# Kernel tuning notes

Measured on AMD Instinct MI355X. Metric: run time of the kernel, lower is better.

## Reference

```python
import jax, jax.numpy as jnp
import numpy as np

N = 50000
E = 600000
IN_C = 128
HID_C = 128
OUT_C = 128


def _glorot(key, shape):
    fan_in, fan_out = shape[0], shape[1]
    lim = np.sqrt(6.0 / (fan_in + fan_out))
    return jax.random.uniform(key, shape, jnp.float32, -lim, lim)


def setup_inputs() -> dict:
    key = jax.random.key(0)
    ks = jax.random.split(key, 10)
    x = jax.random.normal(ks[0], (N, IN_C), jnp.float32)
    edge_index = jax.random.randint(ks[1], (2, E), 0, N, jnp.int64)
    return {
        "x": x,
        "edge_index": edge_index,
        # SAGEConv1: lin_l (aggregated, with bias) and lin_r (root, no bias)
        "W1_l": _glorot(ks[2], (IN_C, HID_C)),
        "b1_l": jnp.zeros((HID_C,), jnp.float32),
        "W1_r": _glorot(ks[3], (IN_C, HID_C)),
        # SAGEConv2
        "W2_l": _glorot(ks[4], (HID_C, OUT_C)),
        "b2_l": jnp.zeros((OUT_C,), jnp.float32),
        "W2_r": _glorot(ks[5], (HID_C, OUT_C)),
        # final Linear(hidden+out -> out)
        "W_lin": _glorot(ks[6], (HID_C + OUT_C, OUT_C)),
        "b_lin": jnp.zeros((OUT_C,), jnp.float32),
    }


def _sage_conv(x, src, dst, W_l, b_l, W_r):
    # mean-aggregate source features onto destination nodes
    msg = x[src]                                   # [E, C] gather
    agg = jax.ops.segment_sum(msg, dst, num_segments=N)        # [N, C]
    cnt = jax.ops.segment_sum(jnp.ones((src.shape[0],), x.dtype), dst,
                              num_segments=N)                   # [N]
    mean = agg / jnp.maximum(cnt, 1.0)[:, None]
    return mean @ W_l + b_l + x @ W_r


def reference(x, edge_index, W1_l, b1_l, W1_r, W2_l, b2_l, W2_r, W_lin, b_lin):
    src, dst = edge_index[0], edge_index[1]
    x1 = jax.nn.relu(_sage_conv(x, src, dst, W1_l, b1_l, W1_r))   # [N, HID]
    x2 = jax.nn.relu(_sage_conv(x1, src, dst, W2_l, b2_l, W2_r))  # [N, OUT]
    return jnp.concatenate([x1, x2], axis=-1) @ W_lin + b_lin     # [N, OUT]
```

## Files before the change

kernel.cpp:

```cpp
#include <hip/hip_runtime.h>


typedef _Float16 f16;
typedef __attribute__((ext_vector_type(2))) _Float16 f16x2;
typedef __attribute__((ext_vector_type(4))) _Float16 f16x4;
typedef __attribute__((ext_vector_type(8))) _Float16 f16x8;
typedef __attribute__((ext_vector_type(4))) float f32x4;

__global__ void convert_f32_to_f16(const float* __restrict__ in, f16* __restrict__ out, int n4) {
  int i = blockIdx.x * blockDim.x + threadIdx.x;
  if (i < n4) {
    const float4 v = ((const float4*)in)[i];
    f16x4 h = { (f16)v.x, (f16)v.y, (f16)v.z, (f16)v.w };
    ((f16x4*)out)[i] = h;
  }
}

__global__ void prep_w(const float* __restrict__ WA, const float* __restrict__ WB,
                       f16* __restrict__ wt) {
  int tid = blockIdx.x * blockDim.x + threadIdx.x;
  if (tid < 32768) {
    int j = tid & 7, n = (tid >> 3) & 127, chunk = tid >> 10;
    int k = chunk * 8 + j;
    float v = (k < 128) ? WA[k * 128 + n] : WB[(k - 128) * 128 + n];
    wt[tid] = (f16)v;
  }
}

__global__ void deg_kernel(const int* __restrict__ ei, int* __restrict__ deg, int E) {
  int e = blockIdx.x * blockDim.x + threadIdx.x;
  if (e < E) atomicAdd(&deg[ei[E + e]], 1);
}

__global__ void scan_block_kernel(const int* __restrict__ in, int* __restrict__ out,
                                  int* __restrict__ sums, int n) {
  __shared__ int s[2][1024];
  int t = threadIdx.x;
  int gid = blockIdx.x * 1024 + t;
  int v = (gid < n) ? in[gid] : 0;
  int cur = 0;
  s[0][t] = v;
  __syncthreads();
  for (int ofs = 1; ofs < 1024; ofs <<= 1) {
    int nv = s[cur][t] + ((t >= ofs) ? s[cur][t - ofs] : 0);
    s[cur ^ 1][t] = nv;
    cur ^= 1;
    __syncthreads();
  }
  if (gid < n) out[gid] = s[cur][t] - v;
  if (t == 1023) sums[blockIdx.x] = s[cur][1023];
}

__global__ void scan_sums_kernel(int* __restrict__ sums, int nb, int* __restrict__ off, int n) {
  int lane = threadIdx.x;
  int orig = (lane < nb) ? sums[lane] : 0;
  int v = orig;
  for (int ofs = 1; ofs < 64; ofs <<= 1) {
    int u = __shfl_up(v, ofs);
    if (lane >= ofs) v += u;
  }
  if (lane < nb) sums[lane] = v - orig;
  if (lane == nb - 1) off[n] = v;
}

__global__ void scan_add_kernel(int* __restrict__ off, const int* __restrict__ sums, int n) {
  int gid = blockIdx.x * 1024 + threadIdx.x;
  if (gid < n) off[gid] += sums[blockIdx.x];
}

__global__ void fill_kernel(const int* __restrict__ ei, const int* __restrict__ off,
                            int* __restrict__ cursor, int* __restrict__ srcs, int E) {
  int e = blockIdx.x * blockDim.x + threadIdx.x;
  if (e < E) {
    int src = ei[e], dst = ei[E + e];
    int pos = atomicAdd(&cursor[dst], 1);
    srcs[off[dst] + pos] = src;
  }
}

__global__ void aggregate_kernel(const f16* __restrict__ feat, const int* __restrict__ off,
                                 const int* __restrict__ srcs, f16* __restrict__ meanf, int n) {
  int wid = (int)((blockIdx.x * blockDim.x + threadIdx.x) >> 6);
  int lane = threadIdx.x & 63;
  if (wid >= n) return;
  int sub = lane >> 4, n15 = lane & 15;
  int beg = off[wid], end = off[wid + 1];
  int deg = end - beg;
  float acc[8] = {};
  int e = beg;
  int bulkEnd = beg + (deg & ~7);
  for (; e < bulkEnd; e += 8) {
    int sA = srcs[e + sub];
    int sB = srcs[e + 4 + sub];
    f16x8 vA = *(const f16x8*)(feat + (size_t)sA * 128 + n15 * 8);
    f16x8 vB = *(const f16x8*)(feat + (size_t)sB * 128 + n15 * 8);
#pragma unroll
    for (int j = 0; j < 8; ++j) acc[j] += (float)vA[j] + (float)vB[j];
  }
  int rem = end - e;
  if (sub < rem) {
    int s = srcs[e + sub];
    f16x8 v = *(const f16x8*)(feat + (size_t)s * 128 + n15 * 8);
#pragma unroll
    for (int j = 0; j < 8; ++j) acc[j] += (float)v[j];
  }
  if (sub + 4 < rem) {
    int s = srcs[e + 4 + sub];
    f16x8 v = *(const f16x8*)(feat + (size_t)s * 128 + n15 * 8);
#pragma unroll
    for (int j = 0; j < 8; ++j) acc[j] += (float)v[j];
  }
#pragma unroll
  for (int j = 0; j < 8; ++j) {
    acc[j] += __shfl_xor(acc[j], 16);
    acc[j] += __shfl_xor(acc[j], 32);
  }
  if (sub == 0) {
    float inv = 1.0f / fmaxf((float)deg, 1.0f);
    f16x8 o;
#pragma unroll
    for (int j = 0; j < 8; ++j) o[j] = (f16)(acc[j] * inv);
    *(f16x8*)(meanf + (size_t)wid * 128 + n15 * 8) = o;
  }
}

template <bool RELU, bool OUT16>
__global__ __launch_bounds__(256, 2) void gemm_kernel(
    const f16* __restrict__ U, const f16* __restrict__ V, const f16* __restrict__ Wt,
    const float* __restrict__ bias, void* __restrict__ outp, int M) {
  __shared__ f16 ldsb[32768];
  int tid = threadIdx.x;
  int wave = tid >> 6, lane = tid & 63;
  int quad = lane >> 4, n15 = lane & 15;
  int m0 = blockIdx.x * 128 + wave * 32;
  int kq = quad * 8;

  f16x8 a[2][8];
#pragma unroll
  for (int r = 0; r < 2; ++r) {
    int row = m0 + r * 16 + n15;
    int rowc = row < M ? row : M - 1;
    const f16* bu = U + (size_t)rowc * 128 + kq;
    const f16* bv = V + (size_t)rowc * 128 + kq;
#pragma unroll
    for (int kk = 0; kk < 4; ++kk) a[r][kk] = *(const f16x8*)(bu + kk * 32);
#pragma unroll
    for (int kk = 4; kk < 8; ++kk) a[r][kk] = *(const f16x8*)(bv + (kk - 4) * 32);
  }

#pragma unroll
  for (int it = 0; it < 16; ++it) {
    int idx = it * 256 + tid;
    ((f16x8*)ldsb)[idx] = ((const f16x8*)Wt)[idx];
  }
  __syncthreads();

  f32x4 acc[2][8] = {};
#pragma unroll
  for (int kk = 0; kk < 8; ++kk) {
#pragma unroll
    for (int t = 0; t < 8; ++t) {
      f16x8 b = ((const f16x8*)ldsb)[(kk * 4 + quad) * 128 + t * 16 + n15];
#pragma unroll
      for (int r = 0; r < 2; ++r)
        acc[r][t] = __builtin_amdgcn_mfma_f32_16x16x32_f16(a[r][kk], b, acc[r][t], 0, 0, 0);
    }
  }

  int rbase0 = m0 + quad * 4;
#pragma unroll
  for (int t = 0; t < 8; ++t) {
    float bv = bias[t * 16 + n15];
#pragma unroll
    for (int r = 0; r < 2; ++r) {
#pragma unroll
      for (int i = 0; i < 4; ++i) {
        int row = rbase0 + r * 16 + i;
        if (row < M) {
          float v = acc[r][t][i] + bv;
          if (RELU) v = fmaxf(v, 0.f);
          size_t idx = (size_t)row * 128 + t * 16 + n15;
          if (OUT16) ((f16*)outp)[idx] = (f16)v;
          else       ((float*)outp)[idx] = v;
        }
      }
    }
  }
}

extern "C" void kernel_launch(void* const* d_in, const int* in_sizes, int n_in,
                              void* d_out, int out_size, void* d_ws, size_t ws_size,
                              hipStream_t stream) {
  (void)n_in; (void)out_size; (void)ws_size;
  const float* x    = (const float*)d_in[0];
  const int*   ei   = (const int*)d_in[1];
  const float* W1l  = (const float*)d_in[2];
  const float* b1l  = (const float*)d_in[3];
  const float* W1r  = (const float*)d_in[4];
  const float* W2l  = (const float*)d_in[5];
  const float* b2l  = (const float*)d_in[6];
  const float* W2r  = (const float*)d_in[7];
  const float* Wlin = (const float*)d_in[8];
  const float* blin = (const float*)d_in[9];
  const int N = in_sizes[0] / 128;
  const int E = in_sizes[1] / 2;

  char* ws = (char*)d_ws;
  size_t o = 0;
  auto alloc = [&](size_t bytes) {
    char* p = ws + o;
    o = (o + bytes + 255) & ~(size_t)255;
    return p;
  };
  f16* xh   = (f16*)alloc((size_t)N * 128 * 2);
  f16* x1h  = (f16*)alloc((size_t)N * 128 * 2);
  f16* x2h  = (f16*)alloc((size_t)N * 128 * 2);
  f16* mh   = (f16*)alloc((size_t)N * 128 * 2);
  f16* wt1  = (f16*)alloc(32768 * 2);
  f16* wt2  = (f16*)alloc(32768 * 2);
  f16* wt3  = (f16*)alloc(32768 * 2);
  int* deg  = (int*)alloc((size_t)N * 2 * 4);
  int* cur  = deg + N;
  int* off  = (int*)alloc(((size_t)N + 1) * 4);
  int* srcs = (int*)alloc((size_t)E * 4);
  int* sums = (int*)alloc(64 * 4);

  hipMemsetAsync(deg, 0, (size_t)N * 2 * 4, stream);

  const int nb = (N + 1023) / 1024;
  deg_kernel<<<(E + 255) / 256, 256, 0, stream>>>(ei, deg, E);
  scan_block_kernel<<<nb, 1024, 0, stream>>>(deg, off, sums, N);
  scan_sums_kernel<<<1, 64, 0, stream>>>(sums, nb, off, N);
  scan_add_kernel<<<nb, 1024, 0, stream>>>(off, sums, N);
  fill_kernel<<<(E + 255) / 256, 256, 0, stream>>>(ei, off, cur, srcs, E);

  convert_f32_to_f16<<<((N * 128 / 4) + 255) / 256, 256, 0, stream>>>(x, xh, N * 128 / 4);
  prep_w<<<128, 256, 0, stream>>>(W1l, W1r, wt1);
  prep_w<<<128, 256, 0, stream>>>(W2l, W2r, wt2);
  prep_w<<<128, 256, 0, stream>>>(Wlin, Wlin + 128 * 128, wt3);

  const int aggBlocks  = (N + 3) / 4;
  const int gemmBlocks = (N + 127) / 128;

  aggregate_kernel<<<aggBlocks, 256, 0, stream>>>(xh, off, srcs, mh, N);
  gemm_kernel<true, true><<<gemmBlocks, 256, 0, stream>>>(mh, xh, wt1, b1l, x1h, N);
  aggregate_kernel<<<aggBlocks, 256, 0, stream>>>(x1h, off, srcs, mh, N);
  gemm_kernel<true, true><<<gemmBlocks, 256, 0, stream>>>(mh, x1h, wt2, b2l, x2h, N);
  gemm_kernel<false, false><<<gemmBlocks, 256, 0, stream>>>(x1h, x2h, wt3, blin, d_out, N);
}
```

Before: 265.1 us.

## Fuse prep kernels, merge scan passes, and batch aggregation two nodes per wave

Merges the x conversion, degree counting and the three weight-repack launches into one multi-role kernel, and folds the scan-sums step into scan_add, which also zeroes the cursor array and writes off[n]=E. This replaces the memset of the cursor and cuts several launches. The aggregation kernel now handles two destination nodes per wave and issues up to six neighbour gathers per node before accumulating, to raise memory-level parallelism. The cost is higher register pressure and more divergence on the remainder path.

```diff
diff --git a/kernel.cpp b/kernel.cpp
--- a/kernel.cpp
+++ b/kernel.cpp
@@ -7,29 +7,34 @@
 typedef __attribute__((ext_vector_type(8))) _Float16 f16x8;
 typedef __attribute__((ext_vector_type(4))) float f32x4;
 
-__global__ void convert_f32_to_f16(const float* __restrict__ in, f16* __restrict__ out, int n4) {
-  int i = blockIdx.x * blockDim.x + threadIdx.x;
-  if (i < n4) {
-    const float4 v = ((const float4*)in)[i];
-    f16x4 h = { (f16)v.x, (f16)v.y, (f16)v.z, (f16)v.w };
-    ((f16x4*)out)[i] = h;
-  }
-}
-
-__global__ void prep_w(const float* __restrict__ WA, const float* __restrict__ WB,
-                       f16* __restrict__ wt) {
-  int tid = blockIdx.x * blockDim.x + threadIdx.x;
-  if (tid < 32768) {
-    int j = tid & 7, n = (tid >> 3) & 127, chunk = tid >> 10;
+__global__ void prep_kernel(const float* __restrict__ x, f16* __restrict__ xh, int n4,
+                            const int* __restrict__ ei, int* __restrict__ deg, int E,
+                            const float* __restrict__ W1l, const float* __restrict__ W1r,
+                            const float* __restrict__ W2l, const float* __restrict__ W2r,
+                            const float* __restrict__ Wlin, f16* __restrict__ wt,
+                            int cb, int db) {
+  int b = blockIdx.x;
+  if (b < cb) {
+    int i = b * 256 + threadIdx.x;
+    if (i < n4) {
+      const float4 v = ((const float4*)x)[i];
+      f16x4 h = { (f16)v.x, (f16)v.y, (f16)v.z, (f16)v.w };
+      ((f16x4*)xh)[i] = h;
+    }
+  } else if (b < cb + db) {
+    int e = (b - cb) * 256 + threadIdx.x;
+    if (e < E) atomicAdd(&deg[ei[E + e]], 1);
+  } else {
+    int tid = (b - cb - db) * 256 + threadIdx.x;
+    int w = tid >> 15, idx = tid & 32767;
+    int j = idx & 7, n = (idx >> 3) & 127, chunk = idx >> 10;
     int k = chunk * 8 + j;
-    float v = (k < 128) ? WA[k * 128 + n] : WB[(k - 128) * 128 + n];
+    float v;
+    if (w == 0) v = (k < 128) ? W1l[k * 128 + n] : W1r[(k - 128) * 128 + n];
+    else if (w == 1) v = (k < 128) ? W2l[k * 128 + n] : W2r[(k - 128) * 128 + n];
+    else v = Wlin[k * 128 + n];
     wt[tid] = (f16)v;
   }
-}
-
-__global__ void deg_kernel(const int* __restrict__ ei, int* __restrict__ deg, int E) {
-  int e = blockIdx.x * blockDim.x + threadIdx.x;
-  if (e < E) atomicAdd(&deg[ei[E + e]], 1);
 }
 
 __global__ void scan_block_kernel(const int* __restrict__ in, int* __restrict__ out,
@@ -51,21 +56,20 @@
   if (t == 1023) sums[blockIdx.x] = s[cur][1023];
 }
 
-__global__ void scan_sums_kernel(int* __restrict__ sums, int nb, int* __restrict__ off, int n) {
-  int lane = threadIdx.x;
-  int orig = (lane < nb) ? sums[lane] : 0;
-  int v = orig;
-  for (int ofs = 1; ofs < 64; ofs <<= 1) {
-    int u = __shfl_up(v, ofs);
-    if (lane >= ofs) v += u;
-  }
-  if (lane < nb) sums[lane] = v - orig;
-  if (lane == nb - 1) off[n] = v;
-}
-
-__global__ void scan_add_kernel(int* __restrict__ off, const int* __restrict__ sums, int n) {
-  int gid = blockIdx.x * 1024 + threadIdx.x;
-  if (gid < n) off[gid] += sums[blockIdx.x];
+__global__ void scan_add_kernel(int* __restrict__ off, const int* __restrict__ sums,
+                                int* __restrict__ cur, int n, int E) {
+  __shared__ int prefix_s;
+  int b = blockIdx.x;
+  if (threadIdx.x < 64) {
+    int v = ((int)threadIdx.x < b) ? sums[threadIdx.x] : 0;
+#pragma unroll
+    for (int ofs = 1; ofs < 64; ofs <<= 1) v += __shfl_xor(v, ofs);
+    if (threadIdx.x == 0) prefix_s = v;
+  }
+  __syncthreads();
+  int gid = b * 1024 + threadIdx.x;
+  if (gid < n) { off[gid] += prefix_s; cur[gid] = 0; }
+  if (gid == 0) off[n] = E;
 }
 
 __global__ void fill_kernel(const int* __restrict__ ei, const int* __restrict__ off,
@@ -78,49 +82,81 @@
   }
 }
 
+#define AGG_R 6
 __global__ void aggregate_kernel(const f16* __restrict__ feat, const int* __restrict__ off,
                                  const int* __restrict__ srcs, f16* __restrict__ meanf, int n) {
-  int wid = (int)((blockIdx.x * blockDim.x + threadIdx.x) >> 6);
+  int pair = (int)((blockIdx.x * blockDim.x + threadIdx.x) >> 6);
+  int w0 = pair * 2;
+  if (w0 >= n) return;
+  int w1 = w0 + 1;
   int lane = threadIdx.x & 63;
-  if (wid >= n) return;
   int sub = lane >> 4, n15 = lane & 15;
-  int beg = off[wid], end = off[wid + 1];
-  int deg = end - beg;
-  float acc[8] = {};
-  int e = beg;
-  int bulkEnd = beg + (deg & ~7);
-  for (; e < bulkEnd; e += 8) {
-    int sA = srcs[e + sub];
-    int sB = srcs[e + 4 + sub];
-    f16x8 vA = *(const f16x8*)(feat + (size_t)sA * 128 + n15 * 8);
-    f16x8 vB = *(const f16x8*)(feat + (size_t)sB * 128 + n15 * 8);
-#pragma unroll
-    for (int j = 0; j < 8; ++j) acc[j] += (float)vA[j] + (float)vB[j];
-  }
-  int rem = end - e;
-  if (sub < rem) {
-    int s = srcs[e + sub];
-    f16x8 v = *(const f16x8*)(feat + (size_t)s * 128 + n15 * 8);
-#pragma unroll
-    for (int j = 0; j < 8; ++j) acc[j] += (float)v[j];
-  }
-  if (sub + 4 < rem) {
-    int s = srcs[e + 4 + sub];
-    f16x8 v = *(const f16x8*)(feat + (size_t)s * 128 + n15 * 8);
-#pragma unroll
-    for (int j = 0; j < 8; ++j) acc[j] += (float)v[j];
+  int beg0 = off[w0], end0 = off[w0 + 1];
+  int beg1 = end0;
+  int end1 = (w1 < n) ? off[w1 + 1] : end0;
+  int deg0 = end0 - beg0, deg1 = end1 - beg1;
+
+  int s0[AGG_R], s1[AGG_R];
+  bool v0[AGG_R], v1[AGG_R];
+#pragma unroll
+  for (int k = 0; k < AGG_R; ++k) {
+    int p = 4 * k + sub;
+    v0[k] = p < deg0;  s0[k] = v0[k] ? srcs[beg0 + p] : 0;
+    v1[k] = p < deg1;  s1[k] = v1[k] ? srcs[beg1 + p] : 0;
+  }
+  f16x8 g0[AGG_R], g1[AGG_R];
+#pragma unroll
+  for (int k = 0; k < AGG_R; ++k) {
+    if (v0[k]) g0[k] = *(const f16x8*)(feat + (size_t)s0[k] * 128 + n15 * 8);
+    if (v1[k]) g1[k] = *(const f16x8*)(feat + (size_t)s1[k] * 128 + n15 * 8);
+  }
+  float acc0[8] = {}, acc1[8] = {};
+#pragma unroll
+  for (int k = 0; k < AGG_R; ++k) {
+    if (v0[k]) {
+#pragma unroll
+      for (int j = 0; j < 8; ++j) acc0[j] += (float)g0[k][j];
+    }
+    if (v1[k]) {
+#pragma unroll
+      for (int j = 0; j < 8; ++j) acc1[j] += (float)g1[k][j];
+    }
+  }
+  for (int e = beg0 + 4 * AGG_R; e < end0; e += 4) {
+    if (sub < end0 - e) {
+      int s = srcs[e + sub];
+      f16x8 g = *(const f16x8*)(feat + (size_t)s * 128 + n15 * 8);
+#pragma unroll
+      for (int j = 0; j < 8; ++j) acc0[j] += (float)g[j];
+    }
+  }
+  for (int e = beg1 + 4 * AGG_R; e < end1; e += 4) {
+    if (sub < end1 - e) {
+      int s = srcs[e + sub];
+      f16x8 g = *(const f16x8*)(feat + (size_t)s * 128 + n15 * 8);
+#pragma unroll
+      for (int j = 0; j < 8; ++j) acc1[j] += (float)g[j];
+    }
   }
 #pragma unroll
   for (int j = 0; j < 8; ++j) {
-    acc[j] += __shfl_xor(acc[j], 16);
-    acc[j] += __shfl_xor(acc[j], 32);
+    acc0[j] += __shfl_xor(acc0[j], 16);
+    acc0[j] += __shfl_xor(acc0[j], 32);
+    acc1[j] += __shfl_xor(acc1[j], 16);
+    acc1[j] += __shfl_xor(acc1[j], 32);
   }
   if (sub == 0) {
-    float inv = 1.0f / fmaxf((float)deg, 1.0f);
+    float inv = 1.0f / fmaxf((float)deg0, 1.0f);
     f16x8 o;
 #pragma unroll
-    for (int j = 0; j < 8; ++j) o[j] = (f16)(acc[j] * inv);
-    *(f16x8*)(meanf + (size_t)wid * 128 + n15 * 8) = o;
+    for (int j = 0; j < 8; ++j) o[j] = (f16)(acc0[j] * inv);
+    *(f16x8*)(meanf + (size_t)w0 * 128 + n15 * 8) = o;
+  } else if (sub == 1 && w1 < n) {
+    float inv = 1.0f / fmaxf((float)deg1, 1.0f);
+    f16x8 o;
+#pragma unroll
+    for (int j = 0; j < 8; ++j) o[j] = (f16)(acc1[j] * inv);
+    *(f16x8*)(meanf + (size_t)w1 * 128 + n15 * 8) = o;
   }
 }
 
@@ -216,30 +252,29 @@
   f16* x1h  = (f16*)alloc((size_t)N * 128 * 2);
   f16* x2h  = (f16*)alloc((size_t)N * 128 * 2);
   f16* mh   = (f16*)alloc((size_t)N * 128 * 2);
-  f16* wt1  = (f16*)alloc(32768 * 2);
-  f16* wt2  = (f16*)alloc(32768 * 2);
-  f16* wt3  = (f16*)alloc(32768 * 2);
-  int* deg  = (int*)alloc((size_t)N * 2 * 4);
-  int* cur  = deg + N;
+  f16* wt   = (f16*)alloc((size_t)3 * 32768 * 2);
+  int* deg  = (int*)alloc((size_t)N * 4);
+  int* cur  = (int*)alloc((size_t)N * 4);
   int* off  = (int*)alloc(((size_t)N + 1) * 4);
   int* srcs = (int*)alloc((size_t)E * 4);
   int* sums = (int*)alloc(64 * 4);
-
-  hipMemsetAsync(deg, 0, (size_t)N * 2 * 4, stream);
+  f16* wt1 = wt, *wt2 = wt + 32768, *wt3 = wt + 65536;
+
+  hipMemsetAsync(deg, 0, (size_t)N * 4, stream);
+
+  const int n4 = N * 128 / 4;
+  const int cb = (n4 + 255) / 256;
+  const int db = (E + 255) / 256;
+  const int wb = (3 * 32768) / 256;
+  prep_kernel<<<cb + db + wb, 256, 0, stream>>>(x, xh, n4, ei, deg, E,
+                                                W1l, W1r, W2l, W2r, Wlin, wt, cb, db);
 
   const int nb = (N + 1023) / 1024;
-  deg_kernel<<<(E + 255) / 256, 256, 0, stream>>>(ei, deg, E);
   scan_block_kernel<<<nb, 1024, 0, stream>>>(deg, off, sums, N);
-  scan_sums_kernel<<<1, 64, 0, stream>>>(sums, nb, off, N);
-  scan_add_kernel<<<nb, 1024, 0, stream>>>(off, sums, N);
-  fill_kernel<<<(E + 255) / 256, 256, 0, stream>>>(ei, off, cur, srcs, E);
-
-  convert_f32_to_f16<<<((N * 128 / 4) + 255) / 256, 256, 0, stream>>>(x, xh, N * 128 / 4);
-  prep_w<<<128, 256, 0, stream>>>(W1l, W1r, wt1);
-  prep_w<<<128, 256, 0, stream>>>(W2l, W2r, wt2);
-  prep_w<<<128, 256, 0, stream>>>(Wlin, Wlin + 128 * 128, wt3);
-
-  const int aggBlocks  = (N + 3) / 4;
+  scan_add_kernel<<<nb, 1024, 0, stream>>>(off, sums, cur, N, E);
+  fill_kernel<<<db, 256, 0, stream>>>(ei, off, cur, srcs, E);
+
+  const int aggBlocks  = ((N + 1) / 2 + 3) / 4;
   const int gemmBlocks = (N + 127) / 128;
 
   aggregate_kernel<<<aggBlocks, 256, 0, stream>>>(xh, off, srcs, mh, N);
```

Measured after the change: 260.6 us. About the same (-1.7%).
